# Performance work log

Hardware: AMD Instinct MI355X
Metric: run time of the kernel (lower is better)

Reference implementation:

```python
import jax, jax.numpy as jnp
import numpy as np
from jax import lax

B, P, GRID, NP = 16, 220, 4, 16
DIM, DEPTH, HEADS, DH, MLP, NC = 512, 6, 8, 64, 2048, 1000
EPS = 1e-5
SCALE = DH ** -0.5
FLAT = 64 * 16 * 16  # per-patch CNN output [64,16,16] flattened (c,p1,p2 order)


def setup_inputs() -> dict:
    key = jax.random.key(0)
    ks = iter(jax.random.split(key, 40))
    def n(shape, std):
        return jax.random.normal(next(ks), shape, dtype=jnp.float32) * std
    return {
        "img": jax.random.normal(next(ks), (B, 1, GRID * P, GRID * P), dtype=jnp.float32),
        "conv1_w": n((32, 1, 7, 7), (2.0 / 49) ** 0.5),
        "conv2_w": n((64, 32, 7, 7), (2.0 / (32 * 49)) ** 0.5),
        "conv3_w": n((64, 64, 7, 7), (2.0 / (64 * 49)) ** 0.5),
        "flat_w": n((FLAT, DIM), FLAT ** -0.5),
        "flat_b": jnp.zeros((DIM,), jnp.float32),
        "cls_token": n((1, 1, DIM), 0.02),
        "pos_emb": n((1, NP + 1, DIM), 0.02),
        "ln1_g": jnp.ones((DEPTH, DIM), jnp.float32),
        "ln1_b": jnp.zeros((DEPTH, DIM), jnp.float32),
        "qkv_w": n((DEPTH, DIM, 3 * HEADS * DH), DIM ** -0.5),
        "out_w": n((DEPTH, HEADS * DH, DIM), (HEADS * DH) ** -0.5),
        "out_b": jnp.zeros((DEPTH, DIM), jnp.float32),
        "ln2_g": jnp.ones((DEPTH, DIM), jnp.float32),
        "ln2_b": jnp.zeros((DEPTH, DIM), jnp.float32),
        "ff1_w": n((DEPTH, DIM, MLP), DIM ** -0.5),
        "ff1_b": jnp.zeros((DEPTH, MLP), jnp.float32),
        "ff2_w": n((DEPTH, MLP, DIM), MLP ** -0.5),
        "ff2_b": jnp.zeros((DEPTH, DIM), jnp.float32),
        "head_ln_g": jnp.ones((DIM,), jnp.float32),
        "head_ln_b": jnp.zeros((DIM,), jnp.float32),
        "head_w": n((DIM, NC), DIM ** -0.5),
        "head_b": jnp.zeros((NC,), jnp.float32),
    }


def _ln(x, g, b):
    m = jnp.mean(x, axis=-1, keepdims=True)
    v = jnp.mean(jnp.square(x - m), axis=-1, keepdims=True)
    return (x - m) * lax.rsqrt(v + EPS) * g + b


def _cnn(x, w1, w2, w3):
    def block(h, w):
        h = lax.conv_general_dilated(h, w, (2, 2), 'VALID',
                                     dimension_numbers=('NCHW', 'OIHW', 'NCHW'))
        h = jax.nn.relu(h)
        # MaxPool2d(kernel=7, stride=1, padding=1)
        return lax.reduce_window(h, -jnp.inf, lax.max, (1, 1, 7, 7), (1, 1, 1, 1),
                                 ((0, 0), (0, 0), (1, 1), (1, 1)))
    return block(block(block(x, w1), w2), w3)


def _forward(img, conv1_w, conv2_w, conv3_w, flat_w, flat_b, cls_token, pos_emb,
             ln1_g, ln1_b, qkv_w, out_w, out_b, ln2_g, ln2_b,
             ff1_w, ff1_b, ff2_w, ff2_b, head_ln_g, head_ln_b, head_w, head_b):
    # b c (h p1) (w p2) -> (b h w) 1 p1 p2 ; all patches batched through the CNN at once
    patches = img.reshape(B, 1, GRID, P, GRID, P).transpose(0, 2, 4, 3, 1, 5)
    patches = patches.reshape(B * NP, 1, P, P)
    feat = _cnn(patches, conv1_w, conv2_w, conv3_w).reshape(B, NP, FLAT)  # [B,NP,64*16*16]
    x = feat @ flat_w + flat_b                                            # [B,NP,DIM]
    x = jnp.concatenate([jnp.broadcast_to(cls_token, (B, 1, DIM)), x], axis=1) + pos_emb
    N = NP + 1

    def layer(x, p):
        g1, b1, qw, ow, ob, g2, b2, w1, fb1, w2, fb2 = p
        h = _ln(x, g1, b1)
        q, k, v = jnp.split(h @ qw, 3, axis=-1)
        def heads(t):
            return t.reshape(B, N, HEADS, DH).transpose(0, 2, 1, 3)  # b h n d
        q, k, v = heads(q), heads(k), heads(v)
        attn = jax.nn.softmax(jnp.einsum('bhqd,bhkd->bhqk', q, k) * SCALE, axis=-1)
        o = jnp.einsum('bhqk,bhkd->bhqd', attn, v).transpose(0, 2, 1, 3).reshape(B, N, HEADS * DH)
        x = x + o @ ow + ob
        h2 = _ln(x, g2, b2)
        x = x + jax.nn.gelu(h2 @ w1 + fb1, approximate=False) @ w2 + fb2
        return x, None

    x, _ = lax.scan(layer, x, (ln1_g, ln1_b, qkv_w, out_w, out_b,
                               ln2_g, ln2_b, ff1_w, ff1_b, ff2_w, ff2_b))
    cls = _ln(x[:, 0], head_ln_g, head_ln_b)
    return cls @ head_w + head_b  # [B, NC]


def reference(img, conv1_w, conv2_w, conv3_w, flat_w, flat_b, cls_token, pos_emb,
              ln1_g, ln1_b, qkv_w, out_w, out_b, ln2_g, ln2_b,
              ff1_w, ff1_b, ff2_w, ff2_b, head_ln_g, head_ln_b, head_w, head_b):
    return _forward(img, conv1_w, conv2_w, conv3_w, flat_w, flat_b, cls_token, pos_emb,
                    ln1_g, ln1_b, qkv_w, out_w, out_b, ln2_g, ln2_b,
                    ff1_w, ff1_b, ff2_w, ff2_b, head_ln_g, head_ln_b, head_w, head_b)
```

## Files before the change

kernel.cpp:

```cpp
#include <hip/hip_runtime.h>
#include <hip/hip_bf16.h>


typedef __hip_bfloat16 bf16;
typedef __attribute__((ext_vector_type(8))) short short8;
typedef __attribute__((ext_vector_type(4))) float floatx4;

#define CHUNK 64

union U8 { int4 v; unsigned short s[8]; };
__device__ inline void umax8(U8& a, const U8& b){
  #pragma unroll
  for (int j = 0; j < 8; j++) a.s[j] = (a.s[j] > b.s[j]) ? a.s[j] : b.s[j];
}
union U4 { uint2 v; unsigned short s[4]; };
__device__ inline void umax4(U4& a, const U4& b){
  #pragma unroll
  for (int j = 0; j < 4; j++) a.s[j] = (a.s[j] > b.s[j]) ? a.s[j] : b.s[j];
}

__global__ __launch_bounds__(256) void prep_w2(const float* __restrict__ w,
                                               bf16* __restrict__ w2b)
{
  int idx = blockIdx.x*256 + threadIdx.x;
  if (idx >= 49*64*32) return;
  int ic = idx & 31; int t = idx >> 5; int oc = t & 63; int kk = t >> 6;
  int ky = kk/7, kx = kk - ky*7;
  w2b[idx] = __float2bfloat16(w[((oc*32+ic)*7+ky)*7+kx]);
}

__global__ __launch_bounds__(256) void prep_w3(const float* __restrict__ w,
                                               bf16* __restrict__ w3b)
{
  int idx = blockIdx.x*256 + threadIdx.x;
  if (idx >= 49*2*64*32) return;
  int ic_l = idx & 31; int t = idx >> 5; int oc = t & 63; int t2 = t >> 6;
  int kx = t2 % 7; int t3 = t2 / 7; int kc = t3 & 1; int ky = t3 >> 1;
  w3b[idx] = __float2bfloat16(w[((oc*64 + kc*32 + ic_l)*7+ky)*7+kx]);
}

__global__ __launch_bounds__(256) void prep_pack(
    const float* __restrict__ src, bf16* __restrict__ dst,
    int K8, int N, int total)
{
  int idx = blockIdx.x*256 + threadIdx.x;
  if (idx >= total) return;
  int n = idx % N; int t = idx / N; int k8 = t % K8; int l = t / K8;
  const float* s = src + ((size_t)l*K8*8 + (size_t)k8*8)*N + n;
  union { bf16 h[8]; int4 v; } pk;
  #pragma unroll
  for (int j = 0; j < 8; j++) pk.h[j] = __float2bfloat16(s[(size_t)j*N]);
  *(int4*)(dst + (((size_t)l*K8 + k8)*N + n)*8) = pk.v;
}

__global__ __launch_bounds__(256) void k1a_conv1(
    const float* __restrict__ img, const float* __restrict__ w,
    bf16* __restrict__ cbuf, int n_base)
{
  __shared__ __align__(16) float in_s[15*224];
  __shared__ float w_s[32*58];
  const int band = blockIdx.x;
  const int n = blockIdx.y;
  const int ng = n_base + n;
  const int r0 = band*5;
  const int ir0 = 2*r0;
  const int b = ng>>4, gh = (ng>>2)&3, gw = ng&3;
  const float* ibase = img + b*774400 + (gh*220)*880 + gw*220;

  for (int idx = threadIdx.x; idx < 15*56; idx += 256){
    int r = idx/56, cq = idx - r*56; int c = cq*4;
    int gr = ir0 + r;
    float4 v = (c < 220 && gr < 220) ? *(const float4*)(ibase + gr*880 + c)
                                     : make_float4(0.f,0.f,0.f,0.f);
    *(float4*)&in_s[r*224 + c] = v;
  }
  for (int idx = threadIdx.x; idx < 32*56; idx += 256){
    int oc = idx/56, k = idx - oc*56; int ky = k>>3, kx = k&7;
    w_s[oc*58 + k] = (kx < 7) ? w[oc*49 + ky*7 + kx] : 0.f;
  }
  __syncthreads();

  const int grp = threadIdx.x & 7;
  const int sp  = threadIdx.x >> 3;
  const int cgc = (sp < 26) ? sp : 26;
  const int nrows = (107 - r0 < 5) ? (107 - r0) : 5;

  float acc[5][4][4] = {};
  #pragma unroll 1
  for (int ky = 0; ky < 7; ky++){
    float wk[4][7];
    #pragma unroll
    for (int oc = 0; oc < 4; oc++)
      #pragma unroll
      for (int kx = 0; kx < 7; kx++)
        wk[oc][kx] = w_s[(grp*4+oc)*58 + ky*8 + kx];
    #pragma unroll
    for (int i = 0; i < 5; i++){
      if (i < nrows){
        const float* ip = &in_s[(2*i+ky)*224 + 8*cgc];
        float iv[13];
        *(float4*)&iv[0] = *(const float4*)ip;
        *(float4*)&iv[4] = *(const float4*)(ip+4);
        *(float4*)&iv[8] = *(const float4*)(ip+8);
        iv[12] = ip[12];
        #pragma unroll
        for (int oc = 0; oc < 4; oc++)
          #pragma unroll
          for (int kx = 0; kx < 7; kx++)
            #pragma unroll
            for (int j = 0; j < 4; j++)
              acc[i][oc][j] += iv[2*j+kx]*wk[oc][kx];
      }
    }
  }

  #pragma unroll
  for (int i = 0; i < 5; i++){
    if (i < nrows){
      int y = r0 + i;
      #pragma unroll
      for (int j = 0; j < 4; j++){
        int col = 4*sp + j;
        if (col < 107){
          union { unsigned short s[4]; uint2 u; } pk;
          #pragma unroll
          for (int oc = 0; oc < 4; oc++){
            bf16 hv = __float2bfloat16(fmaxf(acc[i][oc][j], 0.f));
            pk.s[oc] = *(unsigned short*)&hv;
          }
          *(uint2*)(cbuf + (((size_t)(n*8+grp)*107 + y)*107 + col)*4) = pk.u;
        }
      }
    }
  }
}

__global__ __launch_bounds__(256) void k1b_pool1(
    const bf16* __restrict__ cbuf, bf16* __restrict__ pool1, int n_pool_base)
{
  __shared__ uint2 in4[19*107];
  __shared__ uint2 ht4[19*103];
  const int s = blockIdx.x, g = blockIdx.y, n = blockIdx.z;
  const int p0 = s*13;
  const int PR = (103 - p0 < 13) ? (103 - p0) : 13;
  const int NR = PR + 6;
  const uint2* src = (const uint2*)cbuf + (size_t)(n*8+g)*107*107;

  for (int t = threadIdx.x; t < NR*107; t += 256){
    int r = t/107, c = t - r*107;
    int gr = p0 - 1 + r;
    gr = (gr < 0) ? 0 : ((gr > 106) ? 106 : gr);
    in4[t] = src[gr*107 + c];
  }
  __syncthreads();
  for (int t = threadIdx.x; t < NR*103; t += 256){
    int r = t/103, c = t - r*103;
    U4 m; m.v = in4[r*107 + ((c > 0) ? c-1 : 0)];
    #pragma unroll
    for (int d = 0; d < 6; d++){
      U4 v; v.v = in4[r*107 + ((c+d < 106) ? c+d : 106)];
      umax4(m, v);
    }
    ht4[r*103 + c] = m.v;
  }
  __syncthreads();
  uint2* dst = (uint2*)pool1 + (size_t)((n_pool_base + n)*8 + g)*10609;
  for (int t = threadIdx.x; t < PR*103; t += 256){
    int pr = t/103, c = t - pr*103;
    U4 m; m.v = ht4[pr*103 + c];
    #pragma unroll
    for (int d = 1; d < 7; d++){
      U4 v; v.v = ht4[(pr+d)*103 + c];
      umax4(m, v);
    }
    dst[(p0+pr)*103 + c] = m.v;
  }
}

__global__ __launch_bounds__(256) void k2_conv2(
    const bf16* __restrict__ pool1,
    const bf16* __restrict__ w2b,
    bf16* __restrict__ conv2out)
{
  __shared__ __align__(16) bf16 in_s[7*2*52*40];
  const int n = blockIdx.y, pb = blockIdx.x;
  const int wv = threadIdx.x >> 6, lane = threadIdx.x & 63;
  const int li = lane & 15, lg = lane >> 4;
  const int p0 = pb*256;
  const int y0 = p0/49;

  int pyv[4], pxv[4], poff[4]; bool pmask[4];
  #pragma unroll
  for (int t = 0; t < 4; t++){
    int p = p0 + wv*64 + t*16 + li;
    pmask[t] = (p <= 2400);
    int pc = min(p, 2400);
    int yy = pc/49, xx = pc - yy*49;
    pyv[t] = yy; pxv[t] = xx;
    poff[t] = ((yy - y0)*2*52 + xx)*40;
  }
  floatx4 acc[4][4];
  #pragma unroll
  for (int a = 0; a < 4; a++)
    #pragma unroll
    for (int t = 0; t < 4; t++) acc[a][t] = (floatx4){0.f,0.f,0.f,0.f};

  const unsigned short* pbase = (const unsigned short*)pool1;
  for (int ky = 0; ky < 7; ky++){
    __syncthreads();
    for (int idx = threadIdx.x; idx < 7*103*4; idx += 256){
      int q = idx & 3; int t2 = idx >> 2; int c = t2 % 103; int r = t2/103;
      int gr = min(2*(y0+r)+ky, 102);
      size_t pix = (size_t)gr*103 + c;
      uint2 lov = *(const uint2*)(pbase + (((size_t)n*8 + 2*q  )*10609 + pix)*4);
      uint2 hiv = *(const uint2*)(pbase + (((size_t)n*8 + 2*q+1)*10609 + pix)*4);
      int4 vv; vv.x = (int)lov.x; vv.y = (int)lov.y; vv.z = (int)hiv.x; vv.w = (int)hiv.y;
      *(int4*)&in_s[((r*2 + (c&1))*52 + (c>>1))*40 + q*8] = vv;
    }
    __syncthreads();
    #pragma unroll
    for (int kx = 0; kx < 7; kx++){
      short8 a[4];
      const bf16* wp = w2b + (ky*7+kx)*64*32;
      #pragma unroll
      for (int ot = 0; ot < 4; ot++)
        a[ot] = *(const short8*)(wp + (ot*16 + li)*32 + lg*8);
      int koff = ((kx&1)*52 + (kx>>1))*40 + lg*8;
      #pragma unroll
      for (int t = 0; t < 4; t++){
        short8 bfr = *(const short8*)(&in_s[poff[t] + koff]);
        #pragma unroll
        for (int ot = 0; ot < 4; ot++)
          acc[ot][t] = __builtin_amdgcn_mfma_f32_16x16x32_bf16(a[ot], bfr, acc[ot][t], 0, 0, 0);
      }
    }
  }
  #pragma unroll
  for (int t = 0; t < 4; t++){
    if (!pmask[t]) continue;
    bf16* dst = conv2out + (((long)n*49 + pyv[t])*49 + pxv[t])*64 + lg*4;
    #pragma unroll
    for (int ot = 0; ot < 4; ot++){
      union { bf16 h[4]; uint2 u; } pk;
      #pragma unroll
      for (int v = 0; v < 4; v++)
        pk.h[v] = __float2bfloat16(fmaxf(acc[ot][t][v], 0.f));
      *(uint2*)(dst + ot*16) = pk.u;
    }
  }
}

__global__ __launch_bounds__(256) void k3a_hmax(
    const bf16* __restrict__ cin, bf16* __restrict__ tmp)
{
  int idx = blockIdx.x*256 + threadIdx.x;
  int cg = idx & 7; int t = idx >> 3; int x = t % 45; int t2 = t / 45;
  int y = t2 % 49; int n = t2 / 49;
  const int4* row = (const int4*)(cin + ((long)(n*49 + y)*49)*64) + cg;
  U8 m; m.v = make_int4(0,0,0,0);
  int lo = max(x-1, 0), hi = min(x+5, 48);
  for (int cx = lo; cx <= hi; cx++){ U8 v; v.v = row[cx*8]; umax8(m, v); }
  *((int4*)(tmp + ((long)(n*49 + y)*45 + x)*64) + cg) = m.v;
}

__global__ __launch_bounds__(256) void k3b_vmax(
    const bf16* __restrict__ tmp, bf16* __restrict__ pout, int n_base)
{
  int idx = blockIdx.x*256 + threadIdx.x;
  int cg = idx & 7; int t = idx >> 3; int x = t % 45; int t2 = t / 45;
  int y = t2 % 45; int n = t2 / 45;
  U8 m; m.v = make_int4(0,0,0,0);
  int lo = max(y-1, 0), hi = min(y+5, 48);
  for (int cy = lo; cy <= hi; cy++){
    U8 v; v.v = *((const int4*)(tmp + ((long)(n*49 + cy)*45 + x)*64) + cg);
    umax8(m, v);
  }
  *((int4*)(pout + (long)(n_base+n)*129600 + (y*45 + x)*64) + cg) = m.v;
}

__global__ __launch_bounds__(256) void k4_conv3(
    const bf16* __restrict__ pool2,
    const bf16* __restrict__ w3b,
    bf16* __restrict__ conv3out)
{
  __shared__ __align__(16) bf16 in_s[10*2*24*40];
  const int n = blockIdx.y, pb = blockIdx.x;
  const int wv = threadIdx.x >> 6, lane = threadIdx.x & 63;
  const int li = lane & 15, lg = lane >> 4;
  const int y0 = pb*10;

  int pyv[4], pxv[4], poff[4]; bool pmask[4];
  #pragma unroll
  for (int t = 0; t < 4; t++){
    int pl = wv*64 + t*16 + li;
    pmask[t] = (pl < 200);
    int p = pb*200 + min(pl, 199);
    int yy = p/20, xx = p - yy*20;
    pyv[t] = yy; pxv[t] = xx;
    poff[t] = ((yy - y0)*2*24 + xx)*40;
  }
  floatx4 acc[4][4];
  #pragma unroll
  for (int a = 0; a < 4; a++)
    #pragma unroll
    for (int t = 0; t < 4; t++) acc[a][t] = (floatx4){0.f,0.f,0.f,0.f};

  for (int ky = 0; ky < 7; ky++){
    for (int kc = 0; kc < 2; kc++){
      __syncthreads();
      for (int idx = threadIdx.x; idx < 10*45*4; idx += 256){
        int q = idx & 3; int t2 = idx >> 2; int c = t2 % 45; int r = t2/45;
        int gr = 2*(y0+r)+ky;
        const bf16* src = pool2 + (((long)n*45 + gr)*45 + c)*64 + kc*32 + q*8;
        bf16* dst = &in_s[((r*2 + (c&1))*24 + (c>>1))*40 + q*8];
        *(int4*)dst = *(const int4*)src;
      }
      __syncthreads();
      #pragma unroll
      for (int kx = 0; kx < 7; kx++){
        short8 a[4];
        const bf16* wp = w3b + ((ky*2+kc)*7 + kx)*64*32;
        #pragma unroll
        for (int ot = 0; ot < 4; ot++)
          a[ot] = *(const short8*)(wp + (ot*16 + li)*32 + lg*8);
        int koff = ((kx&1)*24 + (kx>>1))*40 + lg*8;
        #pragma unroll
        for (int t = 0; t < 4; t++){
          short8 bfr = *(const short8*)(&in_s[poff[t] + koff]);
          #pragma unroll
          for (int ot = 0; ot < 4; ot++)
            acc[ot][t] = __builtin_amdgcn_mfma_f32_16x16x32_bf16(a[ot], bfr, acc[ot][t], 0, 0, 0);
        }
      }
    }
  }
  #pragma unroll
  for (int t = 0; t < 4; t++){
    if (!pmask[t]) continue;
    bf16* dst = conv3out + (((long)n*20 + pyv[t])*20 + pxv[t])*64 + lg*4;
    #pragma unroll
    for (int ot = 0; ot < 4; ot++){
      union { bf16 h[4]; uint2 u; } pk;
      #pragma unroll
      for (int v = 0; v < 4; v++)
        pk.h[v] = __float2bfloat16(fmaxf(acc[ot][t][v], 0.f));
      *(uint2*)(dst + ot*16) = pk.u;
    }
  }
}

__global__ __launch_bounds__(256) void k5_pool3(
    const bf16* __restrict__ cin, bf16* __restrict__ feat)
{
  __shared__ int4 in_p[3200];
  __shared__ int4 ht[2560];
  const int n = blockIdx.x;
  const int4* src = (const int4*)(cin + (long)n*25600);
  for (int i = threadIdx.x; i < 3200; i += 256) in_p[i] = src[i];
  __syncthreads();
  for (int i = threadIdx.x; i < 2560; i += 256){
    int cg = i & 7; int t = i >> 3; int x = t & 15; int y = t >> 4;
    U8 m; m.v = make_int4(0,0,0,0);
    int lo = max(x-1, 0), hi = min(x+5, 19);
    for (int cx = lo; cx <= hi; cx++){ U8 v; v.v = in_p[(y*20+cx)*8 + cg]; umax8(m, v); }
    ht[(y*16+x)*8 + cg] = m.v;
  }
  __syncthreads();
  unsigned short* dst = (unsigned short*)(feat + (long)n*16384);
  for (int i = threadIdx.x; i < 2048; i += 256){
    int px = i & 15; int py = (i >> 4) & 15; int cg = i >> 8;
    U8 m; m.v = make_int4(0,0,0,0);
    int lo = max(py-1, 0), hi = min(py+5, 19);
    for (int cy = lo; cy <= hi; cy++){ U8 v; v.v = ht[(cy*16+px)*8 + cg]; umax8(m, v); }
    #pragma unroll
    for (int j = 0; j < 8; j++)
      dst[(cg*8+j)*256 + py*16 + px] = m.s[j];
  }
}

__global__ __launch_bounds__(256) void k6_init_x(
    const float* __restrict__ cls, const float* __restrict__ pos,
    const float* __restrict__ flat_b, float* __restrict__ x)
{
  int idx = blockIdx.x*256 + threadIdx.x;
  int d = idx & 511; int row = idx >> 9;
  int tt = row % 17;
  x[idx] = (tt == 0) ? (cls[d] + pos[d]) : (flat_b[d] + pos[tt*512 + d]);
}

__global__ __launch_bounds__(256) void k6_flat_gemm(
    const bf16* __restrict__ feat, const float* __restrict__ W,
    float* __restrict__ x)
{
  __shared__ float A_s[32][33];
  __shared__ __align__(16) float W_s[32][68];
  const int m0 = blockIdx.x*32, n0 = blockIdx.y*64, ks = blockIdx.z;
  const int r = threadIdx.x>>4, c0 = (threadIdx.x&15)*4;
  float acc0[4] = {}, acc1[4] = {};
  for (int kt = 0; kt < 64; kt++){
    int k0 = ks*2048 + kt*32;
    __syncthreads();
    for (int i = 0; i < 4; i++){ int id = threadIdx.x + i*256; int rr = id>>5, kk = id&31;
      A_s[rr][kk] = __bfloat162float(feat[(long)(m0+rr)*16384 + k0+kk]); }
    for (int i = 0; i < 8; i++){ int id = threadIdx.x + i*256; int kk = id>>6, c = id&63;
      W_s[kk][c] = W[(long)(k0+kk)*512 + n0+c]; }
    __syncthreads();
    #pragma unroll
    for (int kk = 0; kk < 32; kk++){
      float a0 = A_s[r][kk], a1 = A_s[r+16][kk];
      float4 w4 = *(const float4*)&W_s[kk][c0];
      acc0[0]+=a0*w4.x; acc0[1]+=a0*w4.y; acc0[2]+=a0*w4.z; acc0[3]+=a0*w4.w;
      acc1[0]+=a1*w4.x; acc1[1]+=a1*w4.y; acc1[2]+=a1*w4.z; acc1[3]+=a1*w4.w;
    }
  }
  int ma = m0+r, mb = m0+r+16;
  int rowa = (ma>>4)*17 + 1 + (ma&15);
  int rowb = (mb>>4)*17 + 1 + (mb&15);
  for (int j = 0; j < 4; j++){
    atomicAdd(&x[rowa*512 + n0+c0+j], acc0[j]);
    atomicAdd(&x[rowb*512 + n0+c0+j], acc1[j]);
  }
}

__global__ __launch_bounds__(256) void ln_kernel(
    const float* __restrict__ in, const float* __restrict__ g,
    const float* __restrict__ b, float* __restrict__ out,
    int in_stride, int out_stride)
{
  int row = blockIdx.x;
  const float* p = in + (long)row*in_stride;
  float v0 = p[threadIdx.x], v1 = p[threadIdx.x+256];
  __shared__ float red[4]; __shared__ float stat;
  float s = v0+v1;
  #pragma unroll
  for (int o = 32; o >= 1; o >>= 1) s += __shfl_down(s, o);
  int lane = threadIdx.x & 63, wv = threadIdx.x >> 6;
  if (lane == 0) red[wv] = s;
  __syncthreads();
  if (threadIdx.x == 0) stat = (red[0]+red[1]+red[2]+red[3])*(1.0f/512.0f);
  __syncthreads();
  float m = stat;
  float d0 = v0-m, d1 = v1-m;
  float q = d0*d0 + d1*d1;
  #pragma unroll
  for (int o = 32; o >= 1; o >>= 1) q += __shfl_down(q, o);
  __syncthreads();
  if (lane == 0) red[wv] = q;
  __syncthreads();
  if (threadIdx.x == 0) stat = rsqrtf((red[0]+red[1]+red[2]+red[3])*(1.0f/512.0f) + 1e-5f);
  __syncthreads();
  float rstd = stat;
  out[(long)row*out_stride + threadIdx.x]     = d0*rstd*g[threadIdx.x]     + b[threadIdx.x];
  out[(long)row*out_stride + threadIdx.x+256] = d1*rstd*g[threadIdx.x+256] + b[threadIdx.x+256];
}

__global__ __launch_bounds__(256) void ln_bf16(
    const float* __restrict__ in, const float* __restrict__ g,
    const float* __restrict__ b, bf16* __restrict__ out)
{
  int row = blockIdx.x;
  const float* p = in + (long)row*512;
  float v0 = p[threadIdx.x], v1 = p[threadIdx.x+256];
  __shared__ float red[4]; __shared__ float stat;
  float s = v0+v1;
  #pragma unroll
  for (int o = 32; o >= 1; o >>= 1) s += __shfl_down(s, o);
  int lane = threadIdx.x & 63, wv = threadIdx.x >> 6;
  if (lane == 0) red[wv] = s;
  __syncthreads();
  if (threadIdx.x == 0) stat = (red[0]+red[1]+red[2]+red[3])*(1.0f/512.0f);
  __syncthreads();
  float m = stat;
  float d0 = v0-m, d1 = v1-m;
  float q = d0*d0 + d1*d1;
  #pragma unroll
  for (int o = 32; o >= 1; o >>= 1) q += __shfl_down(q, o);
  __syncthreads();
  if (lane == 0) red[wv] = q;
  __syncthreads();
  if (threadIdx.x == 0) stat = rsqrtf((red[0]+red[1]+red[2]+red[3])*(1.0f/512.0f) + 1e-5f);
  __syncthreads();
  float rstd = stat;
  out[(long)row*512 + threadIdx.x]     = __float2bfloat16(d0*rstd*g[threadIdx.x]     + b[threadIdx.x]);
  out[(long)row*512 + threadIdx.x+256] = __float2bfloat16(d1*rstd*g[threadIdx.x+256] + b[threadIdx.x+256]);
}

template<int NT>
__global__ __launch_bounds__(256) void tail_gemm(
    const bf16* __restrict__ A, const bf16* __restrict__ Wp,
    const float* __restrict__ bias, const float* res,
    float* outf, bf16* outb, int N, int K, int dogelu)
{
  const int wv = threadIdx.x >> 6, lane = threadIdx.x & 63;
  const int li = lane & 15, lg = lane >> 4;
  const int m0 = blockIdx.x * 16;
  const int nb = blockIdx.y * (64*NT) + wv * (16*NT);
  floatx4 acc[NT];
  #pragma unroll
  for (int t = 0; t < NT; t++) acc[t] = (floatx4){0.f,0.f,0.f,0.f};
  const bf16* arow = A + (size_t)(m0+li)*K + lg*8;
  for (int k0 = 0; k0 < K; k0 += 32){
    short8 a = *(const short8*)(arow + k0);
    const bf16* wrow = Wp + ((size_t)((k0>>3) + lg) * N + nb + li) * 8;
    #pragma unroll
    for (int t = 0; t < NT; t++){
      short8 bfr = *(const short8*)(wrow + t*128);
      acc[t] = __builtin_amdgcn_mfma_f32_16x16x32_bf16(a, bfr, acc[t], 0, 0, 0);
    }
  }
  #pragma unroll
  for (int t = 0; t < NT; t++){
    int col = nb + t*16 + li;
    #pragma unroll
    for (int v = 0; v < 4; v++){
      int row = m0 + lg*4 + v;
      float val = acc[t][v];
      if (bias) val += bias[col];
      if (dogelu) val = 0.5f*val*(1.0f + erff(val*0.70710678118654752f));
      if (res) val += res[(size_t)row*N + col];
      if (outf) outf[(size_t)row*N + col] = val;
      else      outb[(size_t)row*N + col] = __float2bfloat16(val);
    }
  }
}

__global__ __launch_bounds__(256) void gemm_rows(
    const float* __restrict__ A, const float* __restrict__ W,
    const float* __restrict__ bias, const float* __restrict__ res,
    float* __restrict__ out, int M, int N, int K, int dogelu)
{
  __shared__ float A_s[16][33];
  __shared__ __align__(16) float W_s[32][68];
  const int m0 = blockIdx.x*16, n0 = blockIdx.y*64;
  const int r = threadIdx.x>>4, c0 = (threadIdx.x&15)*4;
  float acc[4] = {};
  for (int k0 = 0; k0 < K; k0 += 32){
    __syncthreads();
    for (int i = 0; i < 2; i++){ int id = threadIdx.x + i*256; int rr = id>>5, kk = id&31;
      A_s[rr][kk] = (m0+rr < M) ? A[(long)(m0+rr)*K + k0+kk] : 0.f; }
    for (int i = 0; i < 8; i++){ int id = threadIdx.x + i*256; int kk = id>>6, c = id&63;
      W_s[kk][c] = (n0+c < N) ? W[(long)(k0+kk)*N + n0+c] : 0.f; }
    __syncthreads();
    #pragma unroll
    for (int kk = 0; kk < 32; kk++){
      float a = A_s[r][kk];
      float4 w4 = *(const float4*)&W_s[kk][c0];
      acc[0]+=a*w4.x; acc[1]+=a*w4.y; acc[2]+=a*w4.z; acc[3]+=a*w4.w;
    }
  }
  if (m0+r < M){
    int row = m0+r;
    for (int j = 0; j < 4; j++){
      int c = n0+c0+j;
      if (c < N){
        float v = acc[j];
        if (bias) v += bias[c];
        if (dogelu) v = 0.5f*v*(1.0f + erff(v*0.70710678118654752f));
        if (res) v += res[(long)row*N + c];
        out[(long)row*N + c] = v;
      }
    }
  }
}

__global__ __launch_bounds__(128) void attn_kernel(
    const float* __restrict__ qkv, bf16* __restrict__ obuf)
{
  const int b = blockIdx.x >> 3, h = blockIdx.x & 7;
  __shared__ float q_s[17][65], k_s[17][65], v_s[17][65], s_s[17][18];
  for (int idx = threadIdx.x; idx < 17*64; idx += 128){
    int i = idx>>6, d = idx&63;
    const float* base = qkv + (long)(b*17+i)*1536 + h*64 + d;
    q_s[i][d] = base[0]; k_s[i][d] = base[512]; v_s[i][d] = base[1024];
  }
  __syncthreads();
  for (int idx = threadIdx.x; idx < 289; idx += 128){
    int i = idx/17, j = idx - i*17;
    float s = 0.f;
    for (int d = 0; d < 64; d++) s += q_s[i][d]*k_s[j][d];
    s_s[i][j] = s*0.125f;
  }
  __syncthreads();
  if (threadIdx.x < 17){
    int i = threadIdx.x;
    float m = -1e30f;
    for (int j = 0; j < 17; j++) m = fmaxf(m, s_s[i][j]);
    float sum = 0.f;
    for (int j = 0; j < 17; j++){ float e = expf(s_s[i][j]-m); s_s[i][j] = e; sum += e; }
    float inv = 1.0f/sum;
    for (int j = 0; j < 17; j++) s_s[i][j] *= inv;
  }
  __syncthreads();
  for (int idx = threadIdx.x; idx < 17*64; idx += 128){
    int i = idx>>6, d = idx&63;
    float o = 0.f;
    for (int j = 0; j < 17; j++) o += s_s[i][j]*v_s[j][d];
    obuf[(long)(b*17+i)*512 + h*64 + d] = __float2bfloat16(o);
  }
}

extern "C" void kernel_launch(void* const* d_in, const int* in_sizes, int n_in,
                              void* d_out, int out_size, void* d_ws, size_t ws_size,
                              hipStream_t stream) {
  const float* img      = (const float*)d_in[0];
  const float* conv1_w  = (const float*)d_in[1];
  const float* conv2_w  = (const float*)d_in[2];
  const float* conv3_w  = (const float*)d_in[3];
  const float* flat_w   = (const float*)d_in[4];
  const float* flat_b   = (const float*)d_in[5];
  const float* cls_tok  = (const float*)d_in[6];
  const float* pos_emb  = (const float*)d_in[7];
  const float* ln1_g    = (const float*)d_in[8];
  const float* ln1_b    = (const float*)d_in[9];
  const float* qkv_w    = (const float*)d_in[10];
  const float* out_w    = (const float*)d_in[11];
  const float* out_b    = (const float*)d_in[12];
  const float* ln2_g    = (const float*)d_in[13];
  const float* ln2_b    = (const float*)d_in[14];
  const float* ff1_w    = (const float*)d_in[15];
  const float* ff1_b    = (const float*)d_in[16];
  const float* ff2_w    = (const float*)d_in[17];
  const float* ff2_b    = (const float*)d_in[18];
  const float* hln_g    = (const float*)d_in[19];
  const float* hln_b    = (const float*)d_in[20];
  const float* head_w   = (const float*)d_in[21];
  const float* head_b   = (const float*)d_in[22];

  char* ws = (char*)d_ws;
  size_t off = 0;
  auto alloc = [&](size_t bytes) -> void* {
    void* p = ws + off; off += (bytes + 255) & ~(size_t)255; return p;
  };
  bf16* pool1    = (bf16*)alloc((size_t)CHUNK*8*103*103*4*2);
  bf16* conv2out = (bf16*)alloc((size_t)CHUNK*49*49*64*2);
  bf16* pool2    = (bf16*)alloc((size_t)256*45*45*64*2);
  bf16* feat     = (bf16*)alloc((size_t)256*16384*2);
  bf16* w2b      = (bf16*)alloc((size_t)49*64*32*2);
  bf16* w3b      = (bf16*)alloc((size_t)49*2*64*32*2);
  float* x       = (float*)alloc((size_t)139264*4);
  bf16*  hb      = (bf16*)alloc((size_t)139264*2);
  float* qkvb    = (float*)alloc((size_t)417792*4);
  bf16*  obufb   = (bf16*)alloc((size_t)139264*2);
  bf16*  ffbufb  = (bf16*)alloc((size_t)557056*2);
  float* hcls    = (float*)alloc((size_t)8192*4);
  bf16* tmp3     = pool1;
  bf16* conv3out = pool1;
  bf16* qkvp  = pool1;
  bf16* outwp = qkvp  + (size_t)6*512*1536;
  bf16* ff1p  = outwp + (size_t)6*512*512;
  bf16* ff2p  = ff1p  + (size_t)6*512*2048;

  const size_t cb_per_n = (size_t)8*107*107*4*2;
  int SUB; bf16* cbuf;
  if (ws_size >= off + 64*cb_per_n)      { SUB = 64; cbuf = (bf16*)alloc(64*cb_per_n); }
  else if (ws_size >= off + 32*cb_per_n) { SUB = 32; cbuf = (bf16*)alloc(32*cb_per_n); }
  else { SUB = 16; cbuf = conv2out; }
  (void)in_sizes; (void)n_in; (void)out_size;

  prep_w2<<<392, 256, 0, stream>>>(conv2_w, w2b);
  prep_w3<<<784, 256, 0, stream>>>(conv3_w, w3b);

  for (int cb = 0; cb < 256; cb += CHUNK){
    for (int sb = 0; sb < CHUNK; sb += SUB){
      k1a_conv1<<<dim3(22, SUB), 256, 0, stream>>>(img, conv1_w, cbuf, cb + sb);
      k1b_pool1<<<dim3(8, 8, SUB), 256, 0, stream>>>(cbuf, pool1, sb);
    }
    k2_conv2     <<<dim3(10,CHUNK), 256, 0, stream>>>(pool1, w2b, conv2out);
    k3a_hmax     <<<(CHUNK*49*45*8)/256, 256, 0, stream>>>(conv2out, tmp3);
    k3b_vmax     <<<(CHUNK*45*45*8)/256, 256, 0, stream>>>(tmp3, pool2, cb);
  }
  k4_conv3<<<dim3(2,256), 256, 0, stream>>>(pool2, w3b, conv3out);
  k5_pool3<<<256, 256, 0, stream>>>(conv3out, feat);

  prep_pack<<<(6*64*1536+255)/256, 256, 0, stream>>>(qkv_w, qkvp, 64, 1536, 6*64*1536);
  prep_pack<<<(6*64*512 +255)/256, 256, 0, stream>>>(out_w, outwp, 64, 512,  6*64*512);
  prep_pack<<<(6*64*2048+255)/256, 256, 0, stream>>>(ff1_w, ff1p, 64, 2048, 6*64*2048);
  prep_pack<<<(6*256*512+255)/256, 256, 0, stream>>>(ff2_w, ff2p, 256, 512, 6*256*512);

  k6_init_x    <<<544,          256, 0, stream>>>(cls_tok, pos_emb, flat_b, x);
  k6_flat_gemm <<<dim3(8,8,8),  256, 0, stream>>>(feat, flat_w, x);

  for (int l = 0; l < 6; l++){
    ln_bf16<<<272, 256, 0, stream>>>(x, ln1_g + l*512, ln1_b + l*512, hb);
    tail_gemm<4><<<dim3(17,6), 256, 0, stream>>>(hb, qkvp + (size_t)l*786432,
                                                 nullptr, nullptr, qkvb, nullptr, 1536, 512, 0);
    attn_kernel<<<128, 128, 0, stream>>>(qkvb, obufb);
    tail_gemm<1><<<dim3(17,8), 256, 0, stream>>>(obufb, outwp + (size_t)l*262144,
                                                 out_b + l*512, x, x, nullptr, 512, 512, 0);
    ln_bf16<<<272, 256, 0, stream>>>(x, ln2_g + l*512, ln2_b + l*512, hb);
    tail_gemm<4><<<dim3(17,8), 256, 0, stream>>>(hb, ff1p + (size_t)l*1048576,
                                                 ff1_b + l*2048, nullptr, nullptr, ffbufb, 2048, 512, 1);
    tail_gemm<1><<<dim3(17,8), 256, 0, stream>>>(ffbufb, ff2p + (size_t)l*1048576,
                                                 ff2_b + l*512, x, x, nullptr, 512, 2048, 0);
  }

  ln_kernel<<<16, 256, 0, stream>>>(x, hln_g, hln_b, hcls, 17*512, 512);
  gemm_rows<<<dim3(1,16), 256, 0, stream>>>(hcls, head_w, head_b, nullptr,
                                            (float*)d_out, 16, 1000, 512, 0);
}
```

Before: 1.742 ms.

## Replace scalar flatten GEMM with bf16 MFMA using hi/lo split weights

Replaces the scalar FP32 shared-memory flatten GEMM with an MFMA 16x16x32 bf16 kernel. The flat_w weight is packed into hi and lo bf16 parts so the weight side keeps near-FP32 accuracy. The packed weights reuse the conv2out and pool2 buffers, which are dead by then. This adds a packing pass over the 32 MB weight and issues two MFMAs per K-step. Operands are loaded straight from global memory without LDS staging.

```diff
diff --git a/kernel.cpp b/kernel.cpp
--- a/kernel.cpp
+++ b/kernel.cpp
@@ -51,6 +51,26 @@
   #pragma unroll
   for (int j = 0; j < 8; j++) pk.h[j] = __float2bfloat16(s[(size_t)j*N]);
   *(int4*)(dst + (((size_t)l*K8 + k8)*N + n)*8) = pk.v;
+}
+
+__global__ __launch_bounds__(256) void prep_pack_flat(
+    const float* __restrict__ src, bf16* __restrict__ hi, bf16* __restrict__ lo)
+{
+  int idx = blockIdx.x*256 + threadIdx.x;
+  if (idx >= 2048*512) return;
+  int n = idx & 511; int k8 = idx >> 9;
+  const float* s = src + (size_t)k8*8*512 + n;
+  union { bf16 h[8]; int4 v; } ph, pl;
+  #pragma unroll
+  for (int j = 0; j < 8; j++){
+    float w = s[(size_t)j*512];
+    bf16 h = __float2bfloat16(w);
+    ph.h[j] = h;
+    pl.h[j] = __float2bfloat16(w - __bfloat162float(h));
+  }
+  size_t o = (size_t)idx*8;
+  *(int4*)(hi + o) = ph.v;
+  *(int4*)(lo + o) = pl.v;
 }
 
 __global__ __launch_bounds__(256) void k1a_conv1(
@@ -388,37 +408,45 @@
   x[idx] = (tt == 0) ? (cls[d] + pos[d]) : (flat_b[d] + pos[tt*512 + d]);
 }
 
-__global__ __launch_bounds__(256) void k6_flat_gemm(
-    const bf16* __restrict__ feat, const float* __restrict__ W,
-    float* __restrict__ x)
-{
-  __shared__ float A_s[32][33];
-  __shared__ __align__(16) float W_s[32][68];
-  const int m0 = blockIdx.x*32, n0 = blockIdx.y*64, ks = blockIdx.z;
-  const int r = threadIdx.x>>4, c0 = (threadIdx.x&15)*4;
-  float acc0[4] = {}, acc1[4] = {};
-  for (int kt = 0; kt < 64; kt++){
-    int k0 = ks*2048 + kt*32;
-    __syncthreads();
-    for (int i = 0; i < 4; i++){ int id = threadIdx.x + i*256; int rr = id>>5, kk = id&31;
-      A_s[rr][kk] = __bfloat162float(feat[(long)(m0+rr)*16384 + k0+kk]); }
-    for (int i = 0; i < 8; i++){ int id = threadIdx.x + i*256; int kk = id>>6, c = id&63;
-      W_s[kk][c] = W[(long)(k0+kk)*512 + n0+c]; }
-    __syncthreads();
-    #pragma unroll
-    for (int kk = 0; kk < 32; kk++){
-      float a0 = A_s[r][kk], a1 = A_s[r+16][kk];
-      float4 w4 = *(const float4*)&W_s[kk][c0];
-      acc0[0]+=a0*w4.x; acc0[1]+=a0*w4.y; acc0[2]+=a0*w4.z; acc0[3]+=a0*w4.w;
-      acc1[0]+=a1*w4.x; acc1[1]+=a1*w4.y; acc1[2]+=a1*w4.z; acc1[3]+=a1*w4.w;
-    }
-  }
-  int ma = m0+r, mb = m0+r+16;
-  int rowa = (ma>>4)*17 + 1 + (ma&15);
-  int rowb = (mb>>4)*17 + 1 + (mb&15);
-  for (int j = 0; j < 4; j++){
-    atomicAdd(&x[rowa*512 + n0+c0+j], acc0[j]);
-    atomicAdd(&x[rowb*512 + n0+c0+j], acc1[j]);
+__global__ __launch_bounds__(256) void k6_flat_mfma(
+    const bf16* __restrict__ feat, const bf16* __restrict__ Whi,
+    const bf16* __restrict__ Wlo, float* __restrict__ x)
+{
+  const int wv = threadIdx.x >> 6, lane = threadIdx.x & 63;
+  const int li = lane & 15, lg = lane >> 4;
+  const int m0 = blockIdx.x*64 + wv*16;
+  const int nb = blockIdx.y*64;
+  const int kb = blockIdx.z*2048;
+  floatx4 acc[4];
+  #pragma unroll
+  for (int t = 0; t < 4; t++) acc[t] = (floatx4){0.f,0.f,0.f,0.f};
+
+  const bf16* arow = feat + (size_t)(m0+li)*16384 + kb + lg*8;
+  for (int k0 = 0; k0 < 2048; k0 += 32){
+    short8 a = *(const short8*)(arow + k0);
+    size_t wo = ((size_t)((kb + k0) >> 3) + lg)*512 + nb + li;
+    const bf16* wh = Whi + wo*8;
+    const bf16* wl = Wlo + wo*8;
+    #pragma unroll
+    for (int t = 0; t < 4; t++){
+      short8 bh = *(const short8*)(wh + t*128);
+      acc[t] = __builtin_amdgcn_mfma_f32_16x16x32_bf16(a, bh, acc[t], 0, 0, 0);
+    }
+    #pragma unroll
+    for (int t = 0; t < 4; t++){
+      short8 bl = *(const short8*)(wl + t*128);
+      acc[t] = __builtin_amdgcn_mfma_f32_16x16x32_bf16(a, bl, acc[t], 0, 0, 0);
+    }
+  }
+  #pragma unroll
+  for (int t = 0; t < 4; t++){
+    int col = nb + t*16 + li;
+    #pragma unroll
+    for (int v = 0; v < 4; v++){
+      int m = m0 + lg*4 + v;
+      int row = (m>>4)*17 + 1 + (m&15);
+      atomicAdd(&x[row*512 + col], acc[t][v]);
+    }
   }
 }
 
@@ -649,6 +677,8 @@
   bf16* outwp = qkvp  + (size_t)6*512*1536;
   bf16* ff1p  = outwp + (size_t)6*512*512;
   bf16* ff2p  = ff1p  + (size_t)6*512*2048;
+  bf16* fwhi  = conv2out;
+  bf16* fwlo  = pool2;
 
   const size_t cb_per_n = (size_t)8*107*107*4*2;
   int SUB; bf16* cbuf;
@@ -672,13 +702,14 @@
   k4_conv3<<<dim3(2,256), 256, 0, stream>>>(pool2, w3b, conv3out);
   k5_pool3<<<256, 256, 0, stream>>>(conv3out, feat);
 
+  prep_pack_flat<<<4096, 256, 0, stream>>>(flat_w, fwhi, fwlo);
   prep_pack<<<(6*64*1536+255)/256, 256, 0, stream>>>(qkv_w, qkvp, 64, 1536, 6*64*1536);
   prep_pack<<<(6*64*512 +255)/256, 256, 0, stream>>>(out_w, outwp, 64, 512,  6*64*512);
   prep_pack<<<(6*64*2048+255)/256, 256, 0, stream>>>(ff1_w, ff1p, 64, 2048, 6*64*2048);
   prep_pack<<<(6*256*512+255)/256, 256, 0, stream>>>(ff2_w, ff2p, 256, 512, 6*256*512);
 
-  k6_init_x    <<<544,          256, 0, stream>>>(cls_tok, pos_emb, flat_b, x);
-  k6_flat_gemm <<<dim3(8,8,8),  256, 0, stream>>>(feat, flat_w, x);
+  k6_init_x    <<<544,         256, 0, stream>>>(cls_tok, pos_emb, flat_b, x);
+  k6_flat_mfma <<<dim3(4,8,8), 256, 0, stream>>>(feat, fwhi, fwlo, x);
 
   for (int l = 0; l < 6; l++){
     ln_bf16<<<272, 256, 0, stream>>>(x, ln1_g + l*512, ln1_b + l*512, hb);
```

Result: no change. 1.720 ms (-1.3%).
